# Kernel optimization log

Measured on AMD Instinct MI355X. Metric: run time of the kernel, lower is better.

Reference implementation:

```python
import jax, jax.numpy as jnp
import numpy as np

B, T, D, H = 4, 2048, 1024, 16
DH = D // H  # 64


def setup_inputs() -> dict:
    key = jax.random.key(0)
    k1, k2, k3 = jax.random.split(key, 3)
    x = jax.random.normal(k1, (B, T, D), dtype=jnp.float32)
    w_qkv = jax.random.normal(k2, (D, 3 * D), dtype=jnp.float32) * (D ** -0.5)
    w_out = jax.random.normal(k3, (D, D), dtype=jnp.float32) * (D ** -0.5)
    return {"x": x, "w_qkv": w_qkv, "w_out": w_out}


def reference(x, w_qkv, w_out):
    b, t, d = x.shape
    qkv = jnp.einsum('btd,de->bte', x, w_qkv)  # [B,T,3D]
    q, k, v = jnp.split(qkv, 3, axis=-1)
    # [B,H,T,DH]
    q = q.reshape(b, t, H, DH).transpose(0, 2, 1, 3)
    k = k.reshape(b, t, H, DH).transpose(0, 2, 1, 3)
    v = v.reshape(b, t, H, DH).transpose(0, 2, 1, 3)
    logits = jnp.einsum('bhqd,bhkd->bhqk', q, k) * (1.0 / jnp.sqrt(jnp.float32(DH)))
    # causal bias: -inf strictly above the diagonal (key index > query index)
    causal = jnp.tril(jnp.ones((t, t), dtype=bool))
    logits = jnp.where(causal, logits, jnp.float32(-jnp.inf))
    scores = jax.nn.softmax(logits, axis=-1)
    y = jnp.einsum('bhqk,bhkd->bhqd', scores, v)
    y = y.transpose(0, 2, 1, 3).reshape(b, t, d)
    return jnp.einsum('btd,de->bte', y, w_out)
```

## Files before the change

### kernel.cpp

```cpp
#include <hip/hip_runtime.h>
#include <hip/hip_bf16.h>


namespace {
constexpr int kB = 4, kT = 2048, kD = 1024, kH = 16;
constexpr int kM = kB * kT;
constexpr int kNq = 3 * kD;
constexpr float kS = 0.180336880f;
}

typedef unsigned short u16;
typedef short bf16x8 __attribute__((ext_vector_type(8)));
typedef float f32x4 __attribute__((ext_vector_type(4)));

__device__ __forceinline__ u16 f2bf(float f) {
  unsigned int u = __float_as_uint(f);
  u += 0x7fffu + ((u >> 16) & 1u);
  return (u16)(u >> 16);
}
__device__ __forceinline__ unsigned int pack2(float a, float b) {
  return (unsigned int)f2bf(a) | ((unsigned int)f2bf(b) << 16);
}
__device__ __forceinline__ unsigned int cvtpk(float a, float b) {
  unsigned int r;
  asm("v_cvt_pk_bf16_f32 %0, %1, %2" : "=v"(r) : "v"(a), "v"(b));
  return r;
}

__device__ __forceinline__ void gload16(const u16* g, u16* l) {
  __builtin_amdgcn_global_load_lds(
      (const __attribute__((address_space(1))) unsigned int*)(uintptr_t)g,
      (__attribute__((address_space(3))) unsigned int*)(uintptr_t)l, 16, 0, 0);
}

__global__ __launch_bounds__(256) void cvt_bf16(const float* __restrict__ x,
                                                u16* __restrict__ xb) {
  const size_t i = ((size_t)blockIdx.x * 256 + threadIdx.x) * 8;
  const float4 v0 = *(const float4*)(x + i);
  const float4 v1 = *(const float4*)(x + i + 4);
  uint4 p;
  p.x = pack2(v0.x, v0.y);
  p.y = pack2(v0.z, v0.w);
  p.z = pack2(v1.x, v1.y);
  p.w = pack2(v1.z, v1.w);
  *(uint4*)(xb + i) = p;
}

__global__ __launch_bounds__(256) void transpose_bf(const float* __restrict__ W,
                                                    u16* __restrict__ WT,
                                                    int K, int N, int nscale) {
  __shared__ float T[32][33];
  const int tid = threadIdx.x;
  const int nb = blockIdx.x * 32, kb = blockIdx.y * 32;
  const int r = tid >> 3, c = (tid & 7) * 4;
  const float4 v = *(const float4*)&W[(size_t)(kb + r) * N + nb + c];
  T[r][c + 0] = v.x;
  T[r][c + 1] = v.y;
  T[r][c + 2] = v.z;
  T[r][c + 3] = v.w;
  __syncthreads();
  const float s = (nb + r < nscale) ? kS : 1.0f;
  uint2 p;
  p.x = pack2(T[c + 0][r] * s, T[c + 1][r] * s);
  p.y = pack2(T[c + 2][r] * s, T[c + 3][r] * s);
  *(uint2*)&WT[(size_t)(nb + r) * K + kb + c] = p;
}

template <bool F32OUT>
__global__ __launch_bounds__(256) void gemm_bt(const u16* __restrict__ A,
                                               const u16* __restrict__ BT,
                                               void* __restrict__ Cv, int lda,
                                               int ldc) {
  __shared__ u16 As[128 * 32];
  __shared__ u16 Bs[128 * 32];
  const int tid = threadIdx.x;
  const int w = tid >> 6, lane = tid & 63;
  const int col = lane & 15, quad = lane >> 4;
  const int wm = (w & 1) * 64, wn = (w >> 1) * 64;
  const int m0 = blockIdx.y * 128, n0 = blockIdx.x * 128;

  const int s0 = tid, s1 = 256 + tid;
  const int ar0 = s0 >> 2, ak0 = ((s0 & 3) ^ ((ar0 >> 1) & 3)) * 8;
  const int ar1 = s1 >> 2, ak1 = ((s1 & 3) ^ ((ar1 >> 1) & 3)) * 8;
  const u16* agp0 = A + (size_t)(m0 + ar0) * lda + ak0;
  const u16* agp1 = A + (size_t)(m0 + ar1) * lda + ak1;
  const u16* bgp0 = BT + (size_t)(n0 + ar0) * kD + ak0;
  const u16* bgp1 = BT + (size_t)(n0 + ar1) * kD + ak1;
  u16* al0 = &As[s0 * 8];
  u16* al1 = &As[s1 * 8];
  u16* bl0 = &Bs[s0 * 8];
  u16* bl1 = &Bs[s1 * 8];

  f32x4 acc[4][4];
#pragma unroll
  for (int mi = 0; mi < 4; ++mi)
#pragma unroll
    for (int ni = 0; ni < 4; ++ni) acc[mi][ni] = (f32x4){0.f, 0.f, 0.f, 0.f};

  for (int k0 = 0; k0 < kD; k0 += 32) {
    __syncthreads();
    gload16(agp0 + k0, al0);
    gload16(agp1 + k0, al1);
    gload16(bgp0 + k0, bl0);
    gload16(bgp1 + k0, bl1);
    __syncthreads();
    bf16x8 af[4], bfr[4];
#pragma unroll
    for (int mi = 0; mi < 4; ++mi) {
      const int r = wm + mi * 16 + col;
      af[mi] = *(const bf16x8*)&As[r * 32 + ((quad ^ ((r >> 1) & 3)) * 8)];
    }
#pragma unroll
    for (int ni = 0; ni < 4; ++ni) {
      const int r = wn + ni * 16 + col;
      bfr[ni] = *(const bf16x8*)&Bs[r * 32 + ((quad ^ ((r >> 1) & 3)) * 8)];
    }
#pragma unroll
    for (int mi = 0; mi < 4; ++mi)
#pragma unroll
      for (int ni = 0; ni < 4; ++ni)
        acc[mi][ni] = __builtin_amdgcn_mfma_f32_16x16x32_bf16(
            af[mi], bfr[ni], acc[mi][ni], 0, 0, 0);
  }

#pragma unroll
  for (int mi = 0; mi < 4; ++mi)
#pragma unroll
    for (int reg = 0; reg < 4; ++reg) {
      const int row = m0 + wm + mi * 16 + quad * 4 + reg;
#pragma unroll
      for (int ni = 0; ni < 4; ++ni) {
        const int cc = n0 + wn + ni * 16 + col;
        if (F32OUT)
          ((float*)Cv)[(size_t)row * ldc + cc] = acc[mi][ni][reg];
        else
          ((u16*)Cv)[(size_t)row * ldc + cc] = f2bf(acc[mi][ni][reg]);
      }
    }
}

__global__ __launch_bounds__(256) void attn_fwd(u16* __restrict__ qkv) {
  __shared__ u16 Ks[2][64 * 64];
  __shared__ u16 Vt[64][72];
  __shared__ u16 Ps[64][72];
  const int tid = threadIdx.x;
  const int w = tid >> 6, lane = tid & 63;
  const int col = lane & 15, quad = lane >> 4;
  const int bh = blockIdx.x;
  const int b = bh >> 4, h = bh & 15;
  const int pa = blockIdx.y;
  const size_t base = (size_t)(b * kT) * kNq + h * 64;

  const int krr = lane >> 3;
  const int ksw = (lane & 7) ^ krr;
  const u16* const kgbase =
      qkv + base + kD + (size_t)(w * 16 + krr) * kNq + ksw * 8;

  const int vkp = (tid & 31) * 2, vd0 = (tid >> 5) * 8;
  const u16* const vgbase = qkv + base + 2 * kD + (size_t)vkp * kNq + vd0;

  bf16x8 onesf;
#pragma unroll
  for (int i = 0; i < 8; ++i) onesf[i] = (short)0x3F80;

  int cur = 0;
#pragma unroll
  for (int pass = 0; pass < 2; ++pass) {
    const int qt = pass ? (31 - pa) : pa;
    const int q0 = qt << 6;

    bf16x8 aq[2];
#pragma unroll
    for (int ks = 0; ks < 2; ++ks)
      aq[ks] = *(const bf16x8*)(qkv + base + (size_t)(q0 + w * 16 + col) * kNq +
                                ks * 32 + quad * 8);

    gload16(kgbase, &Ks[cur][(w * 16) * 64]);
    gload16(kgbase + (size_t)8 * kNq, &Ks[cur][(w * 16 + 8) * 64]);
    uint4 va = *(const uint4*)vgbase;
    uint4 vb = *(const uint4*)(vgbase + kNq);

    f32x4 o[4];
#pragma unroll
    for (int nt = 0; nt < 4; ++nt) o[nt] = (f32x4){0.f, 0.f, 0.f, 0.f};
    f32x4 o4 = (f32x4){0.f, 0.f, 0.f, 0.f};

    for (int kt = 0; kt <= qt; ++kt) {
      __syncthreads();
      {
        const unsigned int* aw = (const unsigned int*)&va;
        const unsigned int* bw = (const unsigned int*)&vb;
#pragma unroll
        for (int i = 0; i < 4; ++i) {
          *(unsigned int*)&Vt[vd0 + 2 * i][vkp] =
              __builtin_amdgcn_perm(bw[i], aw[i], 0x05040100u);
          *(unsigned int*)&Vt[vd0 + 2 * i + 1][vkp] =
              __builtin_amdgcn_perm(bw[i], aw[i], 0x07060302u);
        }
      }
      __syncthreads();

      if (kt < qt) {
        const size_t ko = (size_t)((kt + 1) << 6) * kNq;
        gload16(kgbase + ko, &Ks[cur ^ 1][(w * 16) * 64]);
        gload16(kgbase + ko + (size_t)8 * kNq, &Ks[cur ^ 1][(w * 16 + 8) * 64]);
        va = *(const uint4*)(vgbase + ko);
        vb = *(const uint4*)(vgbase + ko + kNq);
      }

      f32x4 st[4];
#pragma unroll
      for (int nt = 0; nt < 4; ++nt) st[nt] = (f32x4){0.f, 0.f, 0.f, 0.f};
#pragma unroll
      for (int ks = 0; ks < 2; ++ks) {
#pragma unroll
        for (int nt = 0; nt < 4; ++nt) {
          const int kr = nt * 16 + col;
          const bf16x8 bk = *(const bf16x8*)&Ks[cur][kr * 64 +
                                                     (((ks * 4 + quad) ^
                                                       (col & 7)) *
                                                      8)];
          st[nt] = __builtin_amdgcn_mfma_f32_16x16x32_bf16(bk, aq[ks], st[nt],
                                                           0, 0, 0);
        }
      }

      if (kt == qt) {
        const int qrel = w * 16 + col;
#pragma unroll
        for (int nt = 0; nt < 4; ++nt)
#pragma unroll
          for (int reg = 0; reg < 4; ++reg) {
            const int krel = nt * 16 + quad * 4 + reg;
            st[nt][reg] =
                (krel <= qrel) ? __builtin_amdgcn_exp2f(st[nt][reg]) : 0.f;
          }
      } else {
#pragma unroll
        for (int nt = 0; nt < 4; ++nt)
#pragma unroll
          for (int reg = 0; reg < 4; ++reg)
            st[nt][reg] = __builtin_amdgcn_exp2f(st[nt][reg]);
      }

#pragma unroll
      for (int nt = 0; nt < 4; ++nt) {
        uint2 pk;
        pk.x = cvtpk(st[nt][0], st[nt][1]);
        pk.y = cvtpk(st[nt][2], st[nt][3]);
        *(uint2*)&Ps[w * 16 + col][nt * 16 + quad * 4] = pk;
      }

#pragma unroll
      for (int ks = 0; ks < 2; ++ks) {
        const bf16x8 ap =
            *(const bf16x8*)&Ps[w * 16 + col][ks * 32 + quad * 8];
#pragma unroll
        for (int nt = 0; nt < 4; ++nt) {
          const bf16x8 bv =
              *(const bf16x8*)&Vt[nt * 16 + col][ks * 32 + quad * 8];
          o[nt] = __builtin_amdgcn_mfma_f32_16x16x32_bf16(ap, bv, o[nt], 0, 0,
                                                          0);
        }
        o4 = __builtin_amdgcn_mfma_f32_16x16x32_bf16(ap, onesf, o4, 0, 0, 0);
      }
      cur ^= 1;
    }

#pragma unroll
    for (int reg = 0; reg < 4; ++reg) {
      const float inv = 1.0f / o4[reg];
      u16* yp = qkv + base + (size_t)(q0 + w * 16 + quad * 4 + reg) * kNq;
#pragma unroll
      for (int nt = 0; nt < 4; ++nt)
        yp[nt * 16 + col] = f2bf(o[nt][reg] * inv);
    }
  }
}

extern "C" void kernel_launch(void* const* d_in, const int* in_sizes, int n_in,
                              void* d_out, int out_size, void* d_ws,
                              size_t ws_size, hipStream_t stream) {
  const float* x = (const float*)d_in[0];
  const float* w_qkv = (const float*)d_in[1];
  const float* w_out = (const float*)d_in[2];

  u16* wqkvT = (u16*)d_ws;
  u16* woutT = wqkvT + (size_t)kNq * kD;
  u16* qkvb = woutT + (size_t)kD * kD;
  u16* xb = (u16*)d_out;

  cvt_bf16<<<kM * kD / 2048, 256, 0, stream>>>(x, xb);
  transpose_bf<<<dim3(kNq / 32, kD / 32), 256, 0, stream>>>(w_qkv, wqkvT, kD,
                                                            kNq, kD);
  transpose_bf<<<dim3(kD / 32, kD / 32), 256, 0, stream>>>(w_out, woutT, kD,
                                                           kD, 0);
  gemm_bt<false><<<dim3(kNq / 128, kM / 128), 256, 0, stream>>>(xb, wqkvT,
                                                                qkvb, kD, kNq);
  attn_fwd<<<dim3(kB * kH, 16), 256, 0, stream>>>(qkvb);
  gemm_bt<true><<<dim3(kD / 128, kM / 128), 256, 0, stream>>>(qkvb, woutT,
                                                              d_out, kNq, kD);
}
```

Before: 250.0 us.

## Replace QKV projection GEMM with 256x256 double-buffered 8-wave kernel

```diff
diff --git a/kernel.cpp b/kernel.cpp
--- a/kernel.cpp
+++ b/kernel.cpp
@@ -66,6 +66,137 @@
   *(uint2*)&WT[(size_t)(nb + r) * K + kb + c] = p;
 }
 
+__global__ __launch_bounds__(512, 2) void gemm256(const u16* __restrict__ A,
+                                                  const u16* __restrict__ BT,
+                                                  u16* __restrict__ C, int lda,
+                                                  int ldc) {
+  __shared__ u16 As[2][256 * 64];
+  __shared__ u16 Bs[2][256 * 64];
+  constexpr int NT = kD / 64;
+  const int tid = threadIdx.x;
+  const int wid = tid >> 6, lane = tid & 63;
+  const int col = lane & 15, quad = lane >> 4;
+  const int wm_ = wid >> 2, wn_ = wid & 3;
+
+  const int nwg = gridDim.x * gridDim.y;
+  int flat = blockIdx.y * gridDim.x + blockIdx.x;
+  flat = (flat & 7) * (nwg >> 3) + (flat >> 3);
+  const int n0 = (flat % gridDim.x) * 256;
+  const int m0 = (flat / gridDim.x) * 256;
+
+  const int srow = tid >> 3;
+  const int scol8 = (tid & 7) * 8;
+  const int gch8 = ((tid & 7) ^ (srow & 7)) * 8;
+  const u16* const Ag = A + (size_t)(m0 + srow) * lda + gch8;
+  const u16* const Bg = BT + (size_t)(n0 + srow) * kD + gch8;
+
+  f32x4 acc[8][4];
+#pragma unroll
+  for (int i = 0; i < 8; ++i)
+#pragma unroll
+    for (int j = 0; j < 4; ++j) acc[i][j] = (f32x4){0.f, 0.f, 0.f, 0.f};
+
+#define STAGE_A(buf, rbase, k0)                                              \
+  do {                                                                       \
+    gload16(Ag + (size_t)(rbase)*lda + (k0),                                 \
+            &As[buf][((rbase) + srow) * 64 + scol8]);                        \
+    gload16(Ag + (size_t)((rbase) + 64) * lda + (k0),                        \
+            &As[buf][((rbase) + 64 + srow) * 64 + scol8]);                   \
+  } while (0)
+#define STAGE_B(buf, rbase, k0)                                              \
+  do {                                                                       \
+    gload16(Bg + (size_t)(rbase)*kD + (k0),                                  \
+            &Bs[buf][((rbase) + srow) * 64 + scol8]);                        \
+    gload16(Bg + (size_t)((rbase) + 64) * kD + (k0),                         \
+            &Bs[buf][((rbase) + 64 + srow) * 64 + scol8]);                   \
+  } while (0)
+
+  STAGE_A(0, 0, 0);
+  STAGE_B(0, 0, 0);
+  STAGE_B(0, 128, 0);
+  STAGE_A(0, 128, 0);
+  STAGE_A(1, 0, 64);
+  STAGE_B(1, 0, 64);
+  asm volatile("s_waitcnt vmcnt(4)" ::: "memory");
+  __builtin_amdgcn_s_barrier();
+
+  int cur = 0;
+  for (int t = 0; t < NT; ++t) {
+    const int nxt = cur ^ 1;
+#pragma unroll
+    for (int ph = 0; ph < 4; ++ph) {
+      const int mq = ph >> 1, nq = ph & 1;
+      bf16x8 af[4][2], bv[2][2];
+#pragma unroll
+      for (int mi = 0; mi < 4; ++mi) {
+        const int r = mq * 128 + wm_ * 64 + mi * 16 + col;
+#pragma unroll
+        for (int ks = 0; ks < 2; ++ks)
+          af[mi][ks] = *(const bf16x8*)&As[cur][r * 64 +
+                                               (((ks * 4 + quad) ^ (r & 7)) *
+                                                8)];
+      }
+#pragma unroll
+      for (int ni = 0; ni < 2; ++ni) {
+        const int r = nq * 128 + wn_ * 32 + ni * 16 + col;
+#pragma unroll
+        for (int ks = 0; ks < 2; ++ks)
+          bv[ni][ks] = *(const bf16x8*)&Bs[cur][r * 64 +
+                                               (((ks * 4 + quad) ^ (r & 7)) *
+                                                8)];
+      }
+      if (ph == 0) {
+        if (t + 1 < NT) STAGE_B(nxt, 128, (t + 1) * 64);
+      } else if (ph == 1) {
+        if (t + 1 < NT) STAGE_A(nxt, 128, (t + 1) * 64);
+      } else if (ph == 2) {
+        if (t + 2 < NT) STAGE_A(cur, 0, (t + 2) * 64);
+      } else {
+        if (t + 2 < NT) STAGE_B(cur, 0, (t + 2) * 64);
+      }
+      __builtin_amdgcn_s_barrier();
+      asm volatile("s_waitcnt lgkmcnt(0)" ::: "memory");
+      __builtin_amdgcn_s_setprio(1);
+#pragma unroll
+      for (int mi = 0; mi < 4; ++mi)
+#pragma unroll
+        for (int ni = 0; ni < 2; ++ni)
+#pragma unroll
+          for (int ks = 0; ks < 2; ++ks)
+            acc[mq * 4 + mi][nq * 2 + ni] =
+                __builtin_amdgcn_mfma_f32_16x16x32_bf16(
+                    af[mi][ks], bv[ni][ks], acc[mq * 4 + mi][nq * 2 + ni], 0,
+                    0, 0);
+      __builtin_amdgcn_s_setprio(0);
+      if (ph == 3) {
+        if (t + 2 < NT)
+          asm volatile("s_waitcnt vmcnt(4)" ::: "memory");
+        else if (t + 1 < NT)
+          asm volatile("s_waitcnt vmcnt(0)" ::: "memory");
+      }
+      __builtin_amdgcn_s_barrier();
+    }
+    cur = nxt;
+  }
+#undef STAGE_A
+#undef STAGE_B
+
+#pragma unroll
+  for (int mig = 0; mig < 8; ++mig) {
+    const int row =
+        m0 + (mig >> 2) * 128 + wm_ * 64 + (mig & 3) * 16 + quad * 4;
+#pragma unroll
+    for (int reg = 0; reg < 4; ++reg) {
+      u16* cp = C + (size_t)(row + reg) * ldc;
+#pragma unroll
+      for (int nig = 0; nig < 4; ++nig) {
+        const int cc = n0 + (nig >> 1) * 128 + wn_ * 32 + (nig & 1) * 16 + col;
+        cp[cc] = f2bf(acc[mig][nig][reg]);
+      }
+    }
+  }
+}
+
 template <bool F32OUT>
 __global__ __launch_bounds__(256) void gemm_bt(const u16* __restrict__ A,
                                                const u16* __restrict__ BT,
@@ -295,8 +426,8 @@
                                                             kNq, kD);
   transpose_bf<<<dim3(kD / 32, kD / 32), 256, 0, stream>>>(w_out, woutT, kD,
                                                            kD, 0);
-  gemm_bt<false><<<dim3(kNq / 128, kM / 128), 256, 0, stream>>>(xb, wqkvT,
-                                                                qkvb, kD, kNq);
+  gemm256<<<dim3(kNq / 256, kM / 256), 512, 0, stream>>>(xb, wqkvT, qkvb, kD,
+                                                         kNq);
   attn_fwd<<<dim3(kB * kH, 16), 256, 0, stream>>>(qkvb);
   gemm_bt<true><<<dim3(kD / 128, kM / 128), 256, 0, stream>>>(qkvb, woutT,
                                                               d_out, kNq, kD);
```

Result: slower. 257.3 us (+2.9%).

## Rewrite projection GEMMs with 256x128 tiles, double-buffered LDS and XCD-aware block remap

Applied to the files above, without the earlier changes.

```diff
diff --git a/kernel.cpp b/kernel.cpp
--- a/kernel.cpp
+++ b/kernel.cpp
@@ -67,74 +67,149 @@
 }
 
 template <bool F32OUT>
-__global__ __launch_bounds__(256) void gemm_bt(const u16* __restrict__ A,
-                                               const u16* __restrict__ BT,
-                                               void* __restrict__ Cv, int lda,
-                                               int ldc) {
-  __shared__ u16 As[128 * 32];
-  __shared__ u16 Bs[128 * 32];
+__global__ __launch_bounds__(512, 2) void gemm_mt(const u16* __restrict__ A,
+                                                  const u16* __restrict__ BT,
+                                                  void* __restrict__ Cv,
+                                                  int lda, int ldc) {
+  __shared__ u16 As[2][256 * 64];
+  __shared__ u16 Bs[2][128 * 64];
+  constexpr int NT = kD / 64;
   const int tid = threadIdx.x;
-  const int w = tid >> 6, lane = tid & 63;
+  const int wid = tid >> 6, lane = tid & 63;
   const int col = lane & 15, quad = lane >> 4;
-  const int wm = (w & 1) * 64, wn = (w >> 1) * 64;
-  const int m0 = blockIdx.y * 128, n0 = blockIdx.x * 128;
-
-  const int s0 = tid, s1 = 256 + tid;
-  const int ar0 = s0 >> 2, ak0 = ((s0 & 3) ^ ((ar0 >> 1) & 3)) * 8;
-  const int ar1 = s1 >> 2, ak1 = ((s1 & 3) ^ ((ar1 >> 1) & 3)) * 8;
-  const u16* agp0 = A + (size_t)(m0 + ar0) * lda + ak0;
-  const u16* agp1 = A + (size_t)(m0 + ar1) * lda + ak1;
-  const u16* bgp0 = BT + (size_t)(n0 + ar0) * kD + ak0;
-  const u16* bgp1 = BT + (size_t)(n0 + ar1) * kD + ak1;
-  u16* al0 = &As[s0 * 8];
-  u16* al1 = &As[s1 * 8];
-  u16* bl0 = &Bs[s0 * 8];
-  u16* bl1 = &Bs[s1 * 8];
-
-  f32x4 acc[4][4];
-#pragma unroll
-  for (int mi = 0; mi < 4; ++mi)
-#pragma unroll
-    for (int ni = 0; ni < 4; ++ni) acc[mi][ni] = (f32x4){0.f, 0.f, 0.f, 0.f};
-
-  for (int k0 = 0; k0 < kD; k0 += 32) {
-    __syncthreads();
-    gload16(agp0 + k0, al0);
-    gload16(agp1 + k0, al1);
-    gload16(bgp0 + k0, bl0);
-    gload16(bgp1 + k0, bl1);
-    __syncthreads();
-    bf16x8 af[4], bfr[4];
+  const int wm_ = wid >> 2, wn_ = wid & 3;
+
+  const int nwg = gridDim.x * gridDim.y;
+  int flat = blockIdx.y * gridDim.x + blockIdx.x;
+  flat = (flat & 7) * (nwg >> 3) + (flat >> 3);
+  const int n0 = (flat % gridDim.x) * 128;
+  const int m0 = (flat / gridDim.x) * 256;
+
+  const int srow = tid >> 3;
+  const int scol8 = (tid & 7) * 8;
+  const int gch8 = ((tid & 7) ^ (srow & 7)) * 8;
+  const u16* const Ag = A + (size_t)(m0 + srow) * lda + gch8;
+  const u16* const Bg = BT + (size_t)(n0 + srow) * kD + gch8;
+
+  f32x4 acc[8][2];
+#pragma unroll
+  for (int i = 0; i < 8; ++i)
+#pragma unroll
+    for (int j = 0; j < 2; ++j) acc[i][j] = (f32x4){0.f, 0.f, 0.f, 0.f};
+
+#define STAGE_AH(buf, half, k0)                                      \
+  do {                                                               \
+    gload16(Ag + (size_t)((half)*128) * lda + (k0),                  \
+            &As[buf][((half)*128 + srow) * 64 + scol8]);             \
+    gload16(Ag + (size_t)((half)*128 + 64) * lda + (k0),             \
+            &As[buf][((half)*128 + 64 + srow) * 64 + scol8]);        \
+  } while (0)
+#define STAGE_BF(buf, k0)                                            \
+  do {                                                               \
+    gload16(Bg + (size_t)(k0), &Bs[buf][srow * 64 + scol8]);         \
+    gload16(Bg + (size_t)64 * kD + (k0),                             \
+            &Bs[buf][(64 + srow) * 64 + scol8]);                     \
+  } while (0)
+
+  STAGE_AH(0, 0, 0);
+  STAGE_BF(0, 0);
+  STAGE_AH(0, 1, 0);
+  STAGE_AH(1, 0, 64);
+  STAGE_BF(1, 64);
+  asm volatile("s_waitcnt vmcnt(4)" ::: "memory");
+  __builtin_amdgcn_s_barrier();
+
+  for (int t = 0; t < NT; ++t) {
+    const int cur = t & 1;
+    const u16* Ac = &As[cur][0];
+    const u16* Bc = &Bs[cur][0];
+    bf16x8 af[4][2], bv[2][2];
+
 #pragma unroll
     for (int mi = 0; mi < 4; ++mi) {
-      const int r = wm + mi * 16 + col;
-      af[mi] = *(const bf16x8*)&As[r * 32 + ((quad ^ ((r >> 1) & 3)) * 8)];
-    }
-#pragma unroll
-    for (int ni = 0; ni < 4; ++ni) {
-      const int r = wn + ni * 16 + col;
-      bfr[ni] = *(const bf16x8*)&Bs[r * 32 + ((quad ^ ((r >> 1) & 3)) * 8)];
-    }
+      const int r = wm_ * 64 + mi * 16 + col;
+#pragma unroll
+      for (int ks = 0; ks < 2; ++ks)
+        af[mi][ks] =
+            *(const bf16x8*)&Ac[r * 64 + (((ks * 4 + quad) ^ (r & 7)) * 8)];
+    }
+#pragma unroll
+    for (int ni = 0; ni < 2; ++ni) {
+      const int r = wn_ * 32 + ni * 16 + col;
+#pragma unroll
+      for (int ks = 0; ks < 2; ++ks)
+        bv[ni][ks] =
+            *(const bf16x8*)&Bc[r * 64 + (((ks * 4 + quad) ^ (r & 7)) * 8)];
+    }
+    if (t + 1 < NT) STAGE_AH(cur ^ 1, 1, (t + 1) * 64);
+    __builtin_amdgcn_s_barrier();
+    asm volatile("s_waitcnt lgkmcnt(0)" ::: "memory");
+    __builtin_amdgcn_s_setprio(1);
 #pragma unroll
     for (int mi = 0; mi < 4; ++mi)
 #pragma unroll
-      for (int ni = 0; ni < 4; ++ni)
-        acc[mi][ni] = __builtin_amdgcn_mfma_f32_16x16x32_bf16(
-            af[mi], bfr[ni], acc[mi][ni], 0, 0, 0);
+      for (int ni = 0; ni < 2; ++ni)
+#pragma unroll
+        for (int ks = 0; ks < 2; ++ks)
+          acc[mi][ni] = __builtin_amdgcn_mfma_f32_16x16x32_bf16(
+              af[mi][ks], bv[ni][ks], acc[mi][ni], 0, 0, 0);
+    __builtin_amdgcn_s_setprio(0);
+    if (t + 1 < NT)
+      asm volatile("s_waitcnt vmcnt(6)" ::: "memory");
+    else
+      asm volatile("s_waitcnt vmcnt(0)" ::: "memory");
+    __builtin_amdgcn_s_barrier();
+
+#pragma unroll
+    for (int mi = 0; mi < 4; ++mi) {
+      const int r = 128 + wm_ * 64 + mi * 16 + col;
+#pragma unroll
+      for (int ks = 0; ks < 2; ++ks)
+        af[mi][ks] =
+            *(const bf16x8*)&Ac[r * 64 + (((ks * 4 + quad) ^ (r & 7)) * 8)];
+    }
+    if (t + 2 < NT) {
+      STAGE_AH(cur, 0, (t + 2) * 64);
+      STAGE_BF(cur, (t + 2) * 64);
+    }
+    __builtin_amdgcn_s_barrier();
+    asm volatile("s_waitcnt lgkmcnt(0)" ::: "memory");
+    __builtin_amdgcn_s_setprio(1);
+#pragma unroll
+    for (int mi = 0; mi < 4; ++mi)
+#pragma unroll
+      for (int ni = 0; ni < 2; ++ni)
+#pragma unroll
+        for (int ks = 0; ks < 2; ++ks)
+          acc[4 + mi][ni] = __builtin_amdgcn_mfma_f32_16x16x32_bf16(
+              af[mi][ks], bv[ni][ks], acc[4 + mi][ni], 0, 0, 0);
+    __builtin_amdgcn_s_setprio(0);
+    if (t + 2 < NT)
+      asm volatile("s_waitcnt vmcnt(6)" ::: "memory");
+    else if (t + 1 < NT)
+      asm volatile("s_waitcnt vmcnt(2)" ::: "memory");
+    __builtin_amdgcn_s_barrier();
   }
-
-#pragma unroll
-  for (int mi = 0; mi < 4; ++mi)
-#pragma unroll
-    for (int reg = 0; reg < 4; ++reg) {
-      const int row = m0 + wm + mi * 16 + quad * 4 + reg;
-#pragma unroll
-      for (int ni = 0; ni < 4; ++ni) {
-        const int cc = n0 + wn + ni * 16 + col;
-        if (F32OUT)
-          ((float*)Cv)[(size_t)row * ldc + cc] = acc[mi][ni][reg];
-        else
-          ((u16*)Cv)[(size_t)row * ldc + cc] = f2bf(acc[mi][ni][reg]);
+#undef STAGE_AH
+#undef STAGE_BF
+
+#pragma unroll
+  for (int mh = 0; mh < 2; ++mh)
+#pragma unroll
+    for (int mi = 0; mi < 4; ++mi) {
+      const int row = m0 + mh * 128 + wm_ * 64 + mi * 16 + quad * 4;
+#pragma unroll
+      for (int reg = 0; reg < 4; ++reg) {
+#pragma unroll
+        for (int ni = 0; ni < 2; ++ni) {
+          const int cc = n0 + wn_ * 32 + ni * 16 + col;
+          if (F32OUT)
+            ((float*)Cv)[(size_t)(row + reg) * ldc + cc] =
+                acc[mh * 4 + mi][ni][reg];
+          else
+            ((u16*)Cv)[(size_t)(row + reg) * ldc + cc] =
+                f2bf(acc[mh * 4 + mi][ni][reg]);
+        }
       }
     }
 }
@@ -295,9 +370,9 @@
                                                             kNq, kD);
   transpose_bf<<<dim3(kD / 32, kD / 32), 256, 0, stream>>>(w_out, woutT, kD,
                                                            kD, 0);
-  gemm_bt<false><<<dim3(kNq / 128, kM / 128), 256, 0, stream>>>(xb, wqkvT,
+  gemm_mt<false><<<dim3(kNq / 128, kM / 256), 512, 0, stream>>>(xb, wqkvT,
                                                                 qkvb, kD, kNq);
   attn_fwd<<<dim3(kB * kH, 16), 256, 0, stream>>>(qkvb);
-  gemm_bt<true><<<dim3(kD / 128, kM / 128), 256, 0, stream>>>(qkvb, woutT,
+  gemm_mt<true><<<dim3(kD / 128, kM / 256), 512, 0, stream>>>(qkvb, woutT,
                                                               d_out, kNq, kD);
 }
```

Measured after the change: 247.0 us. Within noise of the previous version (-1.2%).
